# Performance work log

Hardware: AMD Instinct MI355X
Metric: run time of the kernel (lower is better)

Reference implementation:

```python
import jax, jax.numpy as jnp
import numpy as np


def setup_inputs() -> dict:
    key = jax.random.key(0)
    k1, k2, k3, k4 = jax.random.split(key, 4)
    B, C_in, E = 8, 32, 100000
    C_out, K = 64, 5
    x = jax.random.normal(k1, (B, C_in, E, 1), dtype=jnp.float32)
    gemm_edges = jax.random.randint(k2, (B, E, 4), 0, E, dtype=jnp.int32)
    fan_in = C_in * K
    weight = jax.random.normal(k3, (C_out, C_in, 1, K), dtype=jnp.float32) / np.sqrt(fan_in)
    bias = jax.random.normal(k4, (C_out,), dtype=jnp.float32) * 0.01
    return {"x": x, "gemm_edges": gemm_edges, "weight": weight, "bias": bias}


def reference(x, gemm_edges, weight, bias):
    # x: (B, C, E, 1) edge features; gemm_edges: (B, E, 4) ring-neighbor indices
    xs = x[..., 0]                                   # (B, C, E)
    B, C, E = xs.shape
    # prepend self index -> (B, E, 5); +1 shifts into padded table (slot 0 = zero pad)
    idx_self = jnp.broadcast_to(jnp.arange(E, dtype=gemm_edges.dtype)[None, :, None], (B, E, 1))
    Gi = jnp.concatenate([idx_self, gemm_edges], axis=2) + 1  # (B, E, 5)
    xp = jnp.pad(xs, ((0, 0), (0, 0), (1, 0)))       # (B, C, E+1) with zero column at index 0
    # per-batch gather: f[b, c, e, k] = xp[b, c, Gi[b, e, k]]
    f = jnp.take_along_axis(xp, Gi.reshape(B, 1, E * 5), axis=2).reshape(B, C, E, 5)
    f0, f1, f2, f3, f4 = (f[..., i] for i in range(5))
    # symmetric functions for neighbor-order invariance
    G = jnp.stack([f0, f1 + f3, f2 + f4, jnp.abs(f1 - f3), jnp.abs(f2 - f4)], axis=3)  # (B, C, E, 5)
    # Conv2d kernel (1, 5) == contraction over (C, k), output (B, C_out, E, 1)
    out = jnp.einsum('bcek,ock->boe', G, weight[:, :, 0, :]) + bias[None, :, None]
    return out[..., None]
```

## Files before the change

### kernel.cpp

```cpp
#include <hip/hip_runtime.h>
#include <stdint.h>

#define E_TOTAL 100000
#define B_TOTAL 8
#define CIN 32
#define COUT 64

typedef short bf16x8 __attribute__((ext_vector_type(8)));
typedef float f32x4 __attribute__((ext_vector_type(4)));

union U16x8 { uint4 u; bf16x8 s; };

__device__ inline float blo(unsigned u) { return __uint_as_float(u << 16); }
__device__ inline float bhi(unsigned u) { return __uint_as_float(u & 0xffff0000u); }
__device__ inline unsigned bpack(float lo, float hi) {
    return (__float_as_uint(lo) >> 16) | (__float_as_uint(hi) & 0xffff0000u);
}
__device__ inline unsigned badd(unsigned a, unsigned b) {
    return bpack(blo(a) + blo(b), bhi(a) + bhi(b));
}
__device__ inline unsigned babsdiff(unsigned a, unsigned b) {
    return bpack(fabsf(blo(a) - blo(b)), fabsf(bhi(a) - bhi(b)));
}
__device__ inline uint4 vadd(uint4 a, uint4 b) {
    uint4 r; r.x = badd(a.x, b.x); r.y = badd(a.y, b.y);
    r.z = badd(a.z, b.z); r.w = badd(a.w, b.w); return r;
}
__device__ inline uint4 vabsdiff(uint4 a, uint4 b) {
    uint4 r; r.x = babsdiff(a.x, b.x); r.y = babsdiff(a.y, b.y);
    r.z = babsdiff(a.z, b.z); r.w = babsdiff(a.w, b.w); return r;
}
__device__ inline unsigned rne16(float f) {
    unsigned b = __float_as_uint(f);
    b += 0x7fffu + ((b >> 16) & 1u);
    return b >> 16;
}

__global__ __launch_bounds__(256) void transpose_cast(
    const float* __restrict__ x, unsigned* __restrict__ xt ) {
    __shared__ float t[CIN][65];
    const int tid = threadIdx.x;
    const int b = blockIdx.x & 7;
    const int e0 = (blockIdx.x >> 3) * 64;
    const int el = tid & 63;
    const int cw = tid >> 6;
#pragma unroll
    for (int i = 0; i < 8; i++) {
        int c = cw * 8 + i;
        int e = e0 + el;
        float v = (e < E_TOTAL) ? x[((size_t)b * CIN + c) * E_TOTAL + e] : 0.f;
        t[c][el] = v;
    }
    __syncthreads();
    const int c2 = tid & 15;
#pragma unroll
    for (int i = 0; i < 4; i++) {
        int el2 = (tid >> 4) * 4 + i;
        int e = e0 + el2;
        if (e < E_TOTAL) {
            unsigned lo = rne16(t[c2 * 2][el2]);
            unsigned hi = rne16(t[c2 * 2 + 1][el2]);
            xt[((size_t)b * E_TOTAL + e) * 16 + c2] = lo | (hi << 16);
        }
    }
}

__global__ void wprep(const float* __restrict__ w, unsigned short* __restrict__ wb) {
    for (int idx = threadIdx.x; idx < 4 * 5 * 64 * 8; idx += 256) {
        int j = idx & 7;
        int lane = (idx >> 3) & 63;
        int tg = idx >> 9;
        int g = tg % 5;
        int t = tg / 5;
        int n = lane & 15, q = lane >> 4;
        int o = n + 16 * t;
        int c = q * 8 + j;
        wb[idx] = (unsigned short)rne16(w[(o * CIN + c) * 5 + g]);
    }
}

__global__ __launch_bounds__(256) void meshconv_main(
    const unsigned short* __restrict__ xt,
    const int* __restrict__ ge,
    const unsigned short* __restrict__ wb,
    const float* __restrict__ bias,
    float* __restrict__ out) {
    const int lane = threadIdx.x & 63;
    const int wv = threadIdx.x >> 6;
    const int b = blockIdx.x & 7;
    const int tile = blockIdx.x >> 3;
    const int e0 = tile * 64 + wv * 16;
    if (e0 >= E_TOTAL) return;
    const int n = lane & 15;
    const int q = lane >> 4;

    uint4 wfrag[4][5];
#pragma unroll
    for (int t = 0; t < 4; t++)
#pragma unroll
        for (int g = 0; g < 5; g++)
            wfrag[t][g] = ((const uint4*)wb)[(t * 5 + g) * 64 + lane];

    int em = e0 + n;
    if (em >= E_TOTAL) em = E_TOTAL - 1;
    const int4 nid = *(const int4*)(ge + ((size_t)b * E_TOTAL + em) * 4);
    const unsigned short* xb = xt + (size_t)b * E_TOTAL * CIN;
    const int co = q * 8;
    uint4 a0 = *(const uint4*)(xb + (size_t)em * CIN + co);
    uint4 a1 = *(const uint4*)(xb + (size_t)nid.x * CIN + co);
    uint4 a2 = *(const uint4*)(xb + (size_t)nid.y * CIN + co);
    uint4 a3 = *(const uint4*)(xb + (size_t)nid.z * CIN + co);
    uint4 a4 = *(const uint4*)(xb + (size_t)nid.w * CIN + co);

    uint4 A[5];
    A[0] = a0;
    A[1] = vadd(a1, a3);
    A[2] = vadd(a2, a4);
    A[3] = vabsdiff(a1, a3);
    A[4] = vabsdiff(a2, a4);

    f32x4 acc[4];
#pragma unroll
    for (int t = 0; t < 4; t++)
#pragma unroll
        for (int r = 0; r < 4; r++) acc[t][r] = 0.f;

#pragma unroll
    for (int g = 0; g < 5; g++) {
        U16x8 av; av.u = A[g];
#pragma unroll
        for (int t = 0; t < 4; t++) {
            U16x8 bv; bv.u = wfrag[t][g];
            acc[t] = __builtin_amdgcn_mfma_f32_16x16x32_bf16(av.s, bv.s, acc[t], 0, 0, 0);
        }
    }

#pragma unroll
    for (int t = 0; t < 4; t++) {
        const int o = n + 16 * t;
        const float bv = bias[o];
        const int ebase = e0 + q * 4;
        float* orow = out + ((size_t)b * COUT + o) * E_TOTAL;
#pragma unroll
        for (int r = 0; r < 4; r++) {
            int e = ebase + r;
            if (e < E_TOTAL) orow[e] = acc[t][r] + bv;
        }
    }
}

__global__ __launch_bounds__(256) void meshconv_fallback(
    const float* __restrict__ x, const int* __restrict__ ge,
    const float* __restrict__ w, const float* __restrict__ bias,
    float* __restrict__ out) {
    __shared__ float f[5][32];
    __shared__ float G[5][32];
    __shared__ int idxs[4];
    const int e = blockIdx.x, b = blockIdx.y;
    const int tid = threadIdx.x;
    if (tid < 4) idxs[tid] = ge[((size_t)b * E_TOTAL + e) * 4 + tid];
    __syncthreads();
    if (tid < 160) {
        int k = tid >> 5, c = tid & 31;
        int src = (k == 0) ? e : idxs[k - 1];
        f[k][c] = x[((size_t)b * CIN + c) * E_TOTAL + src];
    }
    __syncthreads();
    if (tid < 32) {
        int c = tid;
        G[0][c] = f[0][c];
        G[1][c] = f[1][c] + f[3][c];
        G[2][c] = f[2][c] + f[4][c];
        G[3][c] = fabsf(f[1][c] - f[3][c]);
        G[4][c] = fabsf(f[2][c] - f[4][c]);
    }
    __syncthreads();
    if (tid < COUT) {
        float acc = bias[tid];
        for (int c = 0; c < CIN; c++)
#pragma unroll
            for (int g = 0; g < 5; g++)
                acc += G[g][c] * w[(tid * CIN + c) * 5 + g];
        out[((size_t)b * COUT + tid) * E_TOTAL + e] = acc;
    }
}

extern "C" void kernel_launch(void* const* d_in, const int* in_sizes, int n_in,
                              void* d_out, int out_size, void* d_ws, size_t ws_size,
                              hipStream_t stream) {
    const float* x = (const float*)d_in[0];
    const int* ge = (const int*)d_in[1];
    const float* w = (const float*)d_in[2];
    const float* bias = (const float*)d_in[3];
    float* out = (float*)d_out;

    const size_t xt_bytes = (size_t)B_TOTAL * E_TOTAL * CIN * 2;
    const size_t need = 65536 + xt_bytes;
    if (ws_size < need) {
        dim3 grid(E_TOTAL, B_TOTAL);
        meshconv_fallback<<<grid, 256, 0, stream>>>(x, ge, w, bias, out);
        return;
    }
    unsigned short* wb = (unsigned short*)d_ws;
    unsigned short* xt = (unsigned short*)((char*)d_ws + 65536);
    const int tiles = (E_TOTAL + 63) / 64;

    wprep<<<1, 256, 0, stream>>>(w, wb);
    transpose_cast<<<tiles * 8, 256, 0, stream>>>(x, (unsigned*)xt);
    meshconv_main<<<tiles * 8, 256, 0, stream>>>(xt, ge, wb, bias, out);
}
```

Measured before the change: 391.9 us.

## Merge weight prep into transpose kernel, stage weights in LDS, use nontemporal vector I/O

Folds the weight-prep kernel into the transpose kernel as an extra block, which removes one launch. The main kernel now stages bf16 weight fragments in shared memory once per block instead of keeping 20 uint4 fragments per lane in registers, which should ease register pressure and raise occupancy. Input, index and output traffic switches to nontemporal loads and stores, and outputs are written as f32x4 vector stores without a per-element bounds check. The vector store assumes E is a multiple of 4, which holds for 100000, and the weight prep now races with the transpose blocks inside a single launch, which is fine because only the next kernel reads the weights.

```diff
diff --git a/kernel.cpp b/kernel.cpp
--- a/kernel.cpp
+++ b/kernel.cpp
@@ -5,11 +5,14 @@
 #define B_TOTAL 8
 #define CIN 32
 #define COUT 64
+#define TILES 1563
 
 typedef short bf16x8 __attribute__((ext_vector_type(8)));
-typedef float f32x4 __attribute__((ext_vector_type(4)));
-
-union U16x8 { uint4 u; bf16x8 s; };
+typedef float f32x4  __attribute__((ext_vector_type(4)));
+typedef int   i32x4  __attribute__((ext_vector_type(4)));
+typedef unsigned u32x4 __attribute__((ext_vector_type(4)));
+
+union U16x8 { u32x4 u; bf16x8 s; };
 
 __device__ inline float blo(unsigned u) { return __uint_as_float(u << 16); }
 __device__ inline float bhi(unsigned u) { return __uint_as_float(u & 0xffff0000u); }
@@ -22,13 +25,17 @@
 __device__ inline unsigned babsdiff(unsigned a, unsigned b) {
     return bpack(fabsf(blo(a) - blo(b)), fabsf(bhi(a) - bhi(b)));
 }
-__device__ inline uint4 vadd(uint4 a, uint4 b) {
-    uint4 r; r.x = badd(a.x, b.x); r.y = badd(a.y, b.y);
-    r.z = badd(a.z, b.z); r.w = badd(a.w, b.w); return r;
-}
-__device__ inline uint4 vabsdiff(uint4 a, uint4 b) {
-    uint4 r; r.x = babsdiff(a.x, b.x); r.y = babsdiff(a.y, b.y);
-    r.z = babsdiff(a.z, b.z); r.w = babsdiff(a.w, b.w); return r;
+__device__ inline u32x4 vadd4(u32x4 a, u32x4 b) {
+    u32x4 r;
+#pragma unroll
+    for (int i = 0; i < 4; i++) r[i] = badd(a[i], b[i]);
+    return r;
+}
+__device__ inline u32x4 vabsdiff4(u32x4 a, u32x4 b) {
+    u32x4 r;
+#pragma unroll
+    for (int i = 0; i < 4; i++) r[i] = babsdiff(a[i], b[i]);
+    return r;
 }
 __device__ inline unsigned rne16(float f) {
     unsigned b = __float_as_uint(f);
@@ -36,10 +43,25 @@
     return b >> 16;
 }
 
-__global__ __launch_bounds__(256) void transpose_cast(
-    const float* __restrict__ x, unsigned* __restrict__ xt ) {
-    __shared__ float t[CIN][65];
+__global__ __launch_bounds__(256) void prep_transpose(
+    const float* __restrict__ x, unsigned* __restrict__ xt,
+    const float* __restrict__ w, unsigned short* __restrict__ wb) {
     const int tid = threadIdx.x;
+    if (blockIdx.x >= TILES * 8) {
+        for (int idx = tid; idx < 4 * 5 * 64 * 8; idx += 256) {
+            int j = idx & 7;
+            int lane = (idx >> 3) & 63;
+            int tg = idx >> 9;
+            int g = tg % 5;
+            int t = tg / 5;
+            int n = lane & 15, qq = lane >> 4;
+            int o = n + 16 * t;
+            int c = qq * 8 + j;
+            wb[idx] = (unsigned short)rne16(w[(o * CIN + c) * 5 + g]);
+        }
+        return;
+    }
+    __shared__ float tbuf[CIN][65];
     const int b = blockIdx.x & 7;
     const int e0 = (blockIdx.x >> 3) * 64;
     const int el = tid & 63;
@@ -48,8 +70,10 @@
     for (int i = 0; i < 8; i++) {
         int c = cw * 8 + i;
         int e = e0 + el;
-        float v = (e < E_TOTAL) ? x[((size_t)b * CIN + c) * E_TOTAL + e] : 0.f;
-        t[c][el] = v;
+        float v = (e < E_TOTAL)
+            ? __builtin_nontemporal_load(x + ((size_t)b * CIN + c) * E_TOTAL + e)
+            : 0.f;
+        tbuf[c][el] = v;
     }
     __syncthreads();
     const int c2 = tid & 15;
@@ -58,66 +82,52 @@
         int el2 = (tid >> 4) * 4 + i;
         int e = e0 + el2;
         if (e < E_TOTAL) {
-            unsigned lo = rne16(t[c2 * 2][el2]);
-            unsigned hi = rne16(t[c2 * 2 + 1][el2]);
+            unsigned lo = rne16(tbuf[c2 * 2][el2]);
+            unsigned hi = rne16(tbuf[c2 * 2 + 1][el2]);
             xt[((size_t)b * E_TOTAL + e) * 16 + c2] = lo | (hi << 16);
         }
-    }
-}
-
-__global__ void wprep(const float* __restrict__ w, unsigned short* __restrict__ wb) {
-    for (int idx = threadIdx.x; idx < 4 * 5 * 64 * 8; idx += 256) {
-        int j = idx & 7;
-        int lane = (idx >> 3) & 63;
-        int tg = idx >> 9;
-        int g = tg % 5;
-        int t = tg / 5;
-        int n = lane & 15, q = lane >> 4;
-        int o = n + 16 * t;
-        int c = q * 8 + j;
-        wb[idx] = (unsigned short)rne16(w[(o * CIN + c) * 5 + g]);
     }
 }
 
 __global__ __launch_bounds__(256) void meshconv_main(
     const unsigned short* __restrict__ xt,
     const int* __restrict__ ge,
-    const unsigned short* __restrict__ wb,
+    const u32x4* __restrict__ wb,
     const float* __restrict__ bias,
     float* __restrict__ out) {
-    const int lane = threadIdx.x & 63;
-    const int wv = threadIdx.x >> 6;
+    __shared__ u32x4 wlds[1280];
+    const int tid = threadIdx.x;
+    const int lane = tid & 63;
+    const int wv = tid >> 6;
     const int b = blockIdx.x & 7;
     const int tile = blockIdx.x >> 3;
     const int e0 = tile * 64 + wv * 16;
-    if (e0 >= E_TOTAL) return;
     const int n = lane & 15;
     const int q = lane >> 4;
-
-    uint4 wfrag[4][5];
-#pragma unroll
-    for (int t = 0; t < 4; t++)
-#pragma unroll
-        for (int g = 0; g < 5; g++)
-            wfrag[t][g] = ((const uint4*)wb)[(t * 5 + g) * 64 + lane];
-
-    int em = e0 + n;
-    if (em >= E_TOTAL) em = E_TOTAL - 1;
-    const int4 nid = *(const int4*)(ge + ((size_t)b * E_TOTAL + em) * 4);
+    const bool active = (e0 < E_TOTAL);
+    const int em = active ? (e0 + n) : 0;
+
+    i32x4 nid = __builtin_nontemporal_load(
+        (const i32x4*)(ge + ((size_t)b * E_TOTAL + em) * 4));
     const unsigned short* xb = xt + (size_t)b * E_TOTAL * CIN;
     const int co = q * 8;
-    uint4 a0 = *(const uint4*)(xb + (size_t)em * CIN + co);
-    uint4 a1 = *(const uint4*)(xb + (size_t)nid.x * CIN + co);
-    uint4 a2 = *(const uint4*)(xb + (size_t)nid.y * CIN + co);
-    uint4 a3 = *(const uint4*)(xb + (size_t)nid.z * CIN + co);
-    uint4 a4 = *(const uint4*)(xb + (size_t)nid.w * CIN + co);
-
-    uint4 A[5];
+    u32x4 a0 = *(const u32x4*)(xb + (size_t)em * CIN + co);
+
+#pragma unroll
+    for (int k = 0; k < 5; k++) wlds[tid + k * 256] = wb[tid + k * 256];
+    __syncthreads();
+
+    u32x4 a1 = *(const u32x4*)(xb + (size_t)nid[0] * CIN + co);
+    u32x4 a2 = *(const u32x4*)(xb + (size_t)nid[1] * CIN + co);
+    u32x4 a3 = *(const u32x4*)(xb + (size_t)nid[2] * CIN + co);
+    u32x4 a4 = *(const u32x4*)(xb + (size_t)nid[3] * CIN + co);
+
+    u32x4 A[5];
     A[0] = a0;
-    A[1] = vadd(a1, a3);
-    A[2] = vadd(a2, a4);
-    A[3] = vabsdiff(a1, a3);
-    A[4] = vabsdiff(a2, a4);
+    A[1] = vadd4(a1, a3);
+    A[2] = vadd4(a2, a4);
+    A[3] = vabsdiff4(a1, a3);
+    A[4] = vabsdiff4(a2, a4);
 
     f32x4 acc[4];
 #pragma unroll
@@ -130,21 +140,18 @@
         U16x8 av; av.u = A[g];
 #pragma unroll
         for (int t = 0; t < 4; t++) {
-            U16x8 bv; bv.u = wfrag[t][g];
+            U16x8 bv; bv.u = wlds[(t * 5 + g) * 64 + lane];
             acc[t] = __builtin_amdgcn_mfma_f32_16x16x32_bf16(av.s, bv.s, acc[t], 0, 0, 0);
         }
     }
 
-#pragma unroll
-    for (int t = 0; t < 4; t++) {
-        const int o = n + 16 * t;
-        const float bv = bias[o];
-        const int ebase = e0 + q * 4;
-        float* orow = out + ((size_t)b * COUT + o) * E_TOTAL;
-#pragma unroll
-        for (int r = 0; r < 4; r++) {
-            int e = ebase + r;
-            if (e < E_TOTAL) orow[e] = acc[t][r] + bv;
+    if (active) {
+#pragma unroll
+        for (int t = 0; t < 4; t++) {
+            const int o = n + 16 * t;
+            f32x4 r = acc[t] + bias[o];
+            __builtin_nontemporal_store(
+                r, (f32x4*)(out + ((size_t)b * COUT + o) * E_TOTAL + e0 + q * 4));
         }
     }
 }
@@ -203,9 +210,7 @@
     }
     unsigned short* wb = (unsigned short*)d_ws;
     unsigned short* xt = (unsigned short*)((char*)d_ws + 65536);
-    const int tiles = (E_TOTAL + 63) / 64;
-
-    wprep<<<1, 256, 0, stream>>>(w, wb);
-    transpose_cast<<<tiles * 8, 256, 0, stream>>>(x, (unsigned*)xt);
-    meshconv_main<<<tiles * 8, 256, 0, stream>>>(xt, ge, wb, bias, out);
-}
+
+    prep_transpose<<<TILES * 8 + 1, 256, 0, stream>>>(x, (unsigned*)xt, w, wb);
+    meshconv_main<<<TILES * 8, 256, 0, stream>>>(xt, ge, (const u32x4*)wb, bias, out);
+}
```

Measured after the change: 393.2 us. About the same (+0.3%).
